# Optimization experiments

Hardware: AMD Instinct MI355X
Metric: run time of the kernel (lower is better)

Reference implementation:

```python
import jax, jax.numpy as jnp
import numpy as np
import math

RES = 1024
HEADS = 16
HEAD_RES = RES // HEADS
B, S = 2, 2048


def setup_inputs() -> dict:
    key = jax.random.key(0)
    kx, kq, kk, kv = jax.random.split(key, 4)
    scale = 1.0 / math.sqrt(RES)
    return {
        "x": jax.random.normal(kx, (B, S, RES), dtype=jnp.float32),
        "Wq": jax.random.normal(kq, (RES, RES), dtype=jnp.float32) * scale,
        "Wk": jax.random.normal(kk, (RES, RES), dtype=jnp.float32) * scale,
        "Wv": jax.random.normal(kv, (RES, RES), dtype=jnp.float32) * scale,
    }


def reference(x, Wq, Wk, Wv):
    batch, seq, _ = x.shape
    # projections (torch Linear without bias: x @ W.T; here W stored as [in, out])
    def split_heads(t):
        return t.reshape(batch, seq, HEADS, HEAD_RES).transpose(0, 2, 1, 3)  # [B,H,S,D]
    q = split_heads(x @ Wq)
    k = split_heads(x @ Wk)
    v = split_heads(x @ Wv)
    scores = jnp.einsum("bhsd,bhtd->bhst", q, k) / math.sqrt(HEAD_RES)
    attn = jax.nn.softmax(scores, axis=-1)
    out = jnp.einsum("bhst,bhtd->bhsd", attn, v)  # [B,H,S,D]
    return out.transpose(0, 2, 1, 3).reshape(batch, seq, RES)
```

## Files before the change

kernel.cpp:

```cpp
#include <hip/hip_runtime.h>

typedef _Float16 f16;
typedef _Float16 half4 __attribute__((ext_vector_type(4)));
typedef _Float16 half8 __attribute__((ext_vector_type(8)));
typedef float f32x4 __attribute__((ext_vector_type(4)));

#define RES 1024
#define NH 16
#define HD 64
#define BATCH 2
#define SEQ 2048
#define M_ROWS (BATCH * SEQ)

__device__ __forceinline__ void gload_lds16(const void* g, void* l) {
  __builtin_amdgcn_global_load_lds(
      (const __attribute__((address_space(1))) unsigned int*)g,
      (__attribute__((address_space(3))) unsigned int*)l, 16, 0, 0);
}

__global__ __launch_bounds__(256) void xconv_kernel(const float* __restrict__ x,
                                                    f16* __restrict__ xh) {
  int idx = blockIdx.x * 256 + threadIdx.x;
  const float4* xv = (const float4*)x;
  float4 a = xv[idx * 2];
  float4 b = xv[idx * 2 + 1];
  half8 h;
  h[0] = (f16)a.x; h[1] = (f16)a.y; h[2] = (f16)a.z; h[3] = (f16)a.w;
  h[4] = (f16)b.x; h[5] = (f16)b.y; h[6] = (f16)b.z; h[7] = (f16)b.w;
  ((half8*)xh)[idx] = h;
}

__global__ __launch_bounds__(1024) void wtrans_kernel(const float* __restrict__ Wq,
                                                      const float* __restrict__ Wk,
                                                      const float* __restrict__ Wv,
                                                      f16* __restrict__ Wt) {
  const float* W = blockIdx.z == 0 ? Wq : (blockIdx.z == 1 ? Wk : Wv);
  f16* Wo = Wt + (size_t)blockIdx.z * RES * RES;
  __shared__ float tile[32][33];
  int n = blockIdx.x * 32 + threadIdx.x;
  int k = blockIdx.y * 32 + threadIdx.y;
  tile[threadIdx.y][threadIdx.x] = W[(size_t)k * RES + n];
  __syncthreads();
  int ko = blockIdx.y * 32 + threadIdx.x;
  int no = blockIdx.x * 32 + threadIdx.y;
  Wo[(size_t)no * RES + ko] = (f16)tile[threadIdx.x][threadIdx.y];
}

__global__ __launch_bounds__(256) void proj_gemm_kernel(const f16* __restrict__ xh,
                                                        const f16* __restrict__ Wt,
                                                        f16* __restrict__ Qh,
                                                        f16* __restrict__ Kh,
                                                        f16* __restrict__ Vt) {
  int proj = blockIdx.z;
  const f16* Bt = Wt + (size_t)proj * RES * RES;
  int m0 = blockIdx.x * 128;
  int n0 = blockIdx.y * 128;
  __shared__ alignas(16) f16 Als[128 * 32];
  __shared__ alignas(16) f16 Bls[128 * 32];
  int t = threadIdx.x, lane = t & 63, w = t >> 6;
  int l15 = lane & 15, quad = lane >> 4;
  int wm = w >> 1, wn = w & 1;

  f32x4 zero = {0.f, 0.f, 0.f, 0.f};
  f32x4 acc[4][4];
#pragma unroll
  for (int mt = 0; mt < 4; mt++)
#pragma unroll
    for (int nt = 0; nt < 4; nt++) acc[mt][nt] = zero;

  for (int k0 = 0; k0 < RES; k0 += 32) {
#pragma unroll
    for (int i = 0; i < 2; i++) {
      int wl = i * 256 + w * 64;
      int linear = wl + lane;
      int row = linear >> 2;
      int kk = (linear & 3) * 8;
      gload_lds16(xh + (size_t)(m0 + row) * RES + k0 + kk, &Als[wl * 8]);
      gload_lds16(Bt + (size_t)(n0 + row) * RES + k0 + kk, &Bls[wl * 8]);
    }
    __syncthreads();
    half8 af[4], bf[4];
#pragma unroll
    for (int mt = 0; mt < 4; mt++)
      af[mt] = *(const half8*)&Als[(wm * 64 + mt * 16 + l15) * 32 + quad * 8];
#pragma unroll
    for (int nt = 0; nt < 4; nt++)
      bf[nt] = *(const half8*)&Bls[(wn * 64 + nt * 16 + l15) * 32 + quad * 8];
#pragma unroll
    for (int mt = 0; mt < 4; mt++)
#pragma unroll
      for (int nt = 0; nt < 4; nt++)
        acc[mt][nt] = __builtin_amdgcn_mfma_f32_16x16x32_f16(af[mt], bf[nt], acc[mt][nt], 0, 0, 0);
    __syncthreads();
  }

#pragma unroll
  for (int mt = 0; mt < 4; mt++) {
#pragma unroll
    for (int nt = 0; nt < 4; nt++) {
#pragma unroll
      for (int r = 0; r < 4; r++) {
        int row = m0 + wm * 64 + mt * 16 + quad * 4 + r;
        int col = n0 + wn * 64 + nt * 16 + l15;
        f16 v = (f16)acc[mt][nt][r];
        int b = row >> 11, s = row & (SEQ - 1);
        int h = col >> 6, d = col & (HD - 1);
        size_t bh = (size_t)b * NH + h;
        if (proj == 0)
          Qh[(bh * SEQ + s) * HD + d] = v;
        else if (proj == 1)
          Kh[(bh * SEQ + s) * HD + d] = v;
        else
          Vt[(bh * HD + d) * SEQ + s] = v;
      }
    }
  }
}

__global__ __launch_bounds__(128, 3) void flash_kernel(const f16* __restrict__ Qh,
                                                       const f16* __restrict__ Kh,
                                                       const f16* __restrict__ Vt,
                                                       float* __restrict__ out) {
  constexpr int PSTR = 72;
  int L = blockIdx.x;
  int xcd = L & 7, slot = L >> 3;
  int bh = ((slot >> 5) << 3) | xcd;
  int qt = slot & 31;
  int b = bh >> 4, h = bh & 15;
  int tid = threadIdx.x;
  int lane = tid & 63, w = tid >> 6;
  int l15 = lane & 15, quad = lane >> 4;
  int qrow0 = qt * 64 + w * 32;

  __shared__ alignas(16) f16 Kls[64 * 64];
  __shared__ alignas(16) f16 Vls[64 * 64];
  __shared__ alignas(16) f16 p_lds[2][32 * PSTR];

  const f16* kbase = Kh + (size_t)bh * SEQ * HD;
  const f16* vbase = Vt + (size_t)bh * HD * SEQ;

  int srow = tid >> 3;
  int schunk = tid & 7;

  const f16* qptr = Qh + ((size_t)bh * SEQ + qrow0 + l15) * HD + quad * 8;
  half8 qf[2][2];
  qf[0][0] = *(const half8*)qptr;
  qf[0][1] = *(const half8*)(qptr + 32);
  qf[1][0] = *(const half8*)(qptr + 16 * HD);
  qf[1][1] = *(const half8*)(qptr + 16 * HD + 32);
#pragma unroll
  for (int q2 = 0; q2 < 2; q2++)
#pragma unroll
    for (int ks = 0; ks < 2; ks++)
#pragma unroll
      for (int j = 0; j < 8; j++) qf[q2][ks][j] *= (f16)0.125f;

  f32x4 zero = {0.f, 0.f, 0.f, 0.f};
  float l_acc[2] = {0.f, 0.f};
  f32x4 o[2][4];
#pragma unroll
  for (int q2 = 0; q2 < 2; q2++)
#pragma unroll
    for (int nt = 0; nt < 4; nt++) o[q2][nt] = zero;

  int swz0 = (quad ^ (l15 & 7)) * 8;
  int swz1 = ((quad + 4) ^ (l15 & 7)) * 8;

  for (int kv0 = 0; kv0 < SEQ; kv0 += 64) {
#pragma unroll
    for (int rd = 0; rd < 4; rd++) {
      int row = rd * 16 + srow;
      int pc = schunk ^ (row & 7);
      gload_lds16(kbase + ((size_t)(kv0 + row) << 6) + pc * 8,
                  &Kls[rd * 1024 + w * 512]);
      gload_lds16(vbase + ((size_t)row * SEQ) + kv0 + pc * 8,
                  &Vls[rd * 1024 + w * 512]);
    }
    __syncthreads();

    half8 kf0[4], kf1[4];
#pragma unroll
    for (int tt = 0; tt < 4; tt++) {
      int row = tt * 16 + l15;
      kf0[tt] = *(const half8*)&Kls[row * 64 + swz0];
      kf1[tt] = *(const half8*)&Kls[row * 64 + swz1];
    }
#pragma unroll
    for (int q2 = 0; q2 < 2; q2++) {
      f32x4 sc[4];
#pragma unroll
      for (int tt = 0; tt < 4; tt++) {
        sc[tt] = __builtin_amdgcn_mfma_f32_16x16x32_f16(kf0[tt], qf[q2][0], zero, 0, 0, 0);
        sc[tt] = __builtin_amdgcn_mfma_f32_16x16x32_f16(kf1[tt], qf[q2][1], sc[tt], 0, 0, 0);
      }
      float ps = 0.f;
#pragma unroll
      for (int tt = 0; tt < 4; tt++)
#pragma unroll
        for (int r = 0; r < 4; r++) { sc[tt][r] = __expf(sc[tt][r]); ps += sc[tt][r]; }
      ps += __shfl_xor(ps, 16);
      ps += __shfl_xor(ps, 32);
      l_acc[q2] += ps;
#pragma unroll
      for (int tt = 0; tt < 4; tt++) {
        half4 pk;
        pk[0] = (f16)sc[tt][0]; pk[1] = (f16)sc[tt][1];
        pk[2] = (f16)sc[tt][2]; pk[3] = (f16)sc[tt][3];
        *(half4*)&p_lds[w][(q2 * 16 + l15) * PSTR + tt * 16 + quad * 4] = pk;
      }
    }
    half8 vf0[4], vf1[4];
#pragma unroll
    for (int nt = 0; nt < 4; nt++) {
      int row = nt * 16 + l15;
      vf0[nt] = *(const half8*)&Vls[row * 64 + swz0];
      vf1[nt] = *(const half8*)&Vls[row * 64 + swz1];
    }
#pragma unroll
    for (int q2 = 0; q2 < 2; q2++) {
#pragma unroll
      for (int ks = 0; ks < 2; ks++) {
        half8 pf = *(const half8*)&p_lds[w][(q2 * 16 + l15) * PSTR + ks * 32 + quad * 8];
#pragma unroll
        for (int nt = 0; nt < 4; nt++)
          o[q2][nt] = __builtin_amdgcn_mfma_f32_16x16x32_f16(pf, ks ? vf1[nt] : vf0[nt], o[q2][nt], 0, 0, 0);
      }
    }
    __syncthreads();
  }

#pragma unroll
  for (int q2 = 0; q2 < 2; q2++) {
    float linv[4];
#pragma unroll
    for (int r = 0; r < 4; r++) linv[r] = 1.0f / __shfl(l_acc[q2], quad * 4 + r);
#pragma unroll
    for (int nt = 0; nt < 4; nt++) {
#pragma unroll
      for (int r = 0; r < 4; r++) {
        int s = qrow0 + q2 * 16 + quad * 4 + r;
        out[((size_t)b * SEQ + s) * RES + h * HD + nt * 16 + l15] = o[q2][nt][r] * linv[r];
      }
    }
  }
}

extern "C" void kernel_launch(void* const* d_in, const int* in_sizes, int n_in,
                              void* d_out, int out_size, void* d_ws, size_t ws_size,
                              hipStream_t stream) {
  (void)in_sizes; (void)n_in; (void)out_size; (void)ws_size;
  const float* x  = (const float*)d_in[0];
  const float* Wq = (const float*)d_in[1];
  const float* Wk = (const float*)d_in[2];
  const float* Wv = (const float*)d_in[3];
  float* out = (float*)d_out;

  f16* xh = (f16*)d_ws;
  f16* Wt = xh + (size_t)M_ROWS * RES;
  f16* Qh = Wt + (size_t)3 * RES * RES;
  f16* Kh = Qh + (size_t)BATCH * NH * SEQ * HD;
  f16* Vt = Kh + (size_t)BATCH * NH * SEQ * HD;

  xconv_kernel<<<M_ROWS * RES / (256 * 8), 256, 0, stream>>>(x, xh);
  wtrans_kernel<<<dim3(32, 32, 3), dim3(32, 32), 0, stream>>>(Wq, Wk, Wv, Wt);
  proj_gemm_kernel<<<dim3(M_ROWS / 128, RES / 128, 3), 256, 0, stream>>>(xh, Wt, Qh, Kh, Vt);
  flash_kernel<<<1024, 128, 0, stream>>>(Qh, Kh, Vt, out);
}
```

Measured before the change: 172.5 us.

## Keep softmax probabilities in registers via permlane swaps and prefetch next KV tile

```diff
diff --git a/kernel.cpp b/kernel.cpp
--- a/kernel.cpp
+++ b/kernel.cpp
@@ -1,9 +1,9 @@
 #include <hip/hip_runtime.h>
 
 typedef _Float16 f16;
-typedef _Float16 half4 __attribute__((ext_vector_type(4)));
 typedef _Float16 half8 __attribute__((ext_vector_type(8)));
 typedef float f32x4 __attribute__((ext_vector_type(4)));
+typedef unsigned int u32x4 __attribute__((ext_vector_type(4)));
 
 #define RES 1024
 #define NH 16
@@ -16,6 +16,37 @@
   __builtin_amdgcn_global_load_lds(
       (const __attribute__((address_space(1))) unsigned int*)g,
       (__attribute__((address_space(3))) unsigned int*)l, 16, 0, 0);
+}
+
+__device__ __forceinline__ unsigned pk16(float a, float b) {
+  auto h = __builtin_amdgcn_cvt_pkrtz(a, b);
+  return __builtin_bit_cast(unsigned, h);
+}
+
+__device__ __forceinline__ void swap32(unsigned a, unsigned b, unsigned& x, unsigned& y) {
+#if __has_builtin(__builtin_amdgcn_permlane32_swap)
+  auto t = __builtin_amdgcn_permlane32_swap(a, b, false, false);
+  x = (unsigned)t[0];
+  y = (unsigned)t[1];
+#else
+  unsigned ax = __shfl_xor(a, 32), bx = __shfl_xor(b, 32);
+  int hi = (threadIdx.x & 63) >> 5;
+  x = hi ? bx : a;
+  y = hi ? b : ax;
+#endif
+}
+
+__device__ __forceinline__ void swap16(unsigned a, unsigned b, unsigned& x, unsigned& y) {
+#if __has_builtin(__builtin_amdgcn_permlane16_swap)
+  auto t = __builtin_amdgcn_permlane16_swap(a, b, false, false);
+  x = (unsigned)t[0];
+  y = (unsigned)t[1];
+#else
+  unsigned ax = __shfl_xor(a, 16), bx = __shfl_xor(b, 16);
+  int q1 = ((threadIdx.x & 63) >> 4) & 1;
+  x = q1 ? bx : a;
+  y = q1 ? b : ax;
+#endif
 }
 
 __global__ __launch_bounds__(256) void xconv_kernel(const float* __restrict__ x,
@@ -121,7 +152,6 @@
                                                        const f16* __restrict__ Kh,
                                                        const f16* __restrict__ Vt,
                                                        float* __restrict__ out) {
-  constexpr int PSTR = 72;
   int L = blockIdx.x;
   int xcd = L & 7, slot = L >> 3;
   int bh = ((slot >> 5) << 3) | xcd;
@@ -134,7 +164,6 @@
 
   __shared__ alignas(16) f16 Kls[64 * 64];
   __shared__ alignas(16) f16 Vls[64 * 64];
-  __shared__ alignas(16) f16 p_lds[2][32 * PSTR];
 
   const f16* kbase = Kh + (size_t)bh * SEQ * HD;
   const f16* vbase = Vt + (size_t)bh * HD * SEQ;
@@ -166,7 +195,7 @@
   int swz0 = (quad ^ (l15 & 7)) * 8;
   int swz1 = ((quad + 4) ^ (l15 & 7)) * 8;
 
-  for (int kv0 = 0; kv0 < SEQ; kv0 += 64) {
+  auto stage = [&](int kv0) {
 #pragma unroll
     for (int rd = 0; rd < 4; rd++) {
       int row = rd * 16 + srow;
@@ -176,6 +205,11 @@
       gload_lds16(vbase + ((size_t)row * SEQ) + kv0 + pc * 8,
                   &Vls[rd * 1024 + w * 512]);
     }
+  };
+
+  stage(0);
+
+  for (int kv0 = 0; kv0 < SEQ; kv0 += 64) {
     __syncthreads();
 
     half8 kf0[4], kf1[4];
@@ -185,6 +219,8 @@
       kf0[tt] = *(const half8*)&Kls[row * 64 + swz0];
       kf1[tt] = *(const half8*)&Kls[row * 64 + swz1];
     }
+
+    half8 pa[2][2];
 #pragma unroll
     for (int q2 = 0; q2 < 2; q2++) {
       f32x4 sc[4];
@@ -201,14 +237,28 @@
       ps += __shfl_xor(ps, 16);
       ps += __shfl_xor(ps, 32);
       l_acc[q2] += ps;
+
+      unsigned wp[4][2];
 #pragma unroll
       for (int tt = 0; tt < 4; tt++) {
-        half4 pk;
-        pk[0] = (f16)sc[tt][0]; pk[1] = (f16)sc[tt][1];
-        pk[2] = (f16)sc[tt][2]; pk[3] = (f16)sc[tt][3];
-        *(half4*)&p_lds[w][(q2 * 16 + l15) * PSTR + tt * 16 + quad * 4] = pk;
-      }
-    }
+        wp[tt][0] = pk16(sc[tt][0], sc[tt][1]);
+        wp[tt][1] = pk16(sc[tt][2], sc[tt][3]);
+      }
+#pragma unroll
+      for (int ks = 0; ks < 2; ks++) {
+        u32x4 pw;
+#pragma unroll
+        for (int i = 0; i < 2; i++) {
+          unsigned a, bb, x, y;
+          swap32(wp[2 * ks][i], wp[2 * ks + 1][i], a, bb);
+          swap16(a, bb, x, y);
+          pw[i] = x;
+          pw[2 + i] = y;
+        }
+        pa[q2][ks] = __builtin_bit_cast(half8, pw);
+      }
+    }
+
     half8 vf0[4], vf1[4];
 #pragma unroll
     for (int nt = 0; nt < 4; nt++) {
@@ -216,17 +266,18 @@
       vf0[nt] = *(const half8*)&Vls[row * 64 + swz0];
       vf1[nt] = *(const half8*)&Vls[row * 64 + swz1];
     }
-#pragma unroll
-    for (int q2 = 0; q2 < 2; q2++) {
-#pragma unroll
-      for (int ks = 0; ks < 2; ks++) {
-        half8 pf = *(const half8*)&p_lds[w][(q2 * 16 + l15) * PSTR + ks * 32 + quad * 8];
+
+    __syncthreads();
+
+    if (kv0 + 64 < SEQ) stage(kv0 + 64);
+
+#pragma unroll
+    for (int q2 = 0; q2 < 2; q2++)
+#pragma unroll
+      for (int ks = 0; ks < 2; ks++)
 #pragma unroll
         for (int nt = 0; nt < 4; nt++)
-          o[q2][nt] = __builtin_amdgcn_mfma_f32_16x16x32_f16(pf, ks ? vf1[nt] : vf0[nt], o[q2][nt], 0, 0, 0);
-      }
-    }
-    __syncthreads();
+          o[q2][nt] = __builtin_amdgcn_mfma_f32_16x16x32_f16(pa[q2][ks], ks ? vf1[nt] : vf0[nt], o[q2][nt], 0, 0, 0);
   }
 
 #pragma unroll
```

After: 169.3 us, median of 3. No clear change (-1.9%).
